# Kernel optimization log

Measured on AMD Instinct MI355X. Metric: run time of the kernel, lower is better.

## Reference

```python
import jax, jax.numpy as jnp
import numpy as np

T, B, DIN, H, DM, HYP, L = 128, 512, 512, 512, 256, 256, 100
STDV = 1.0 / np.sqrt(H)  # reset_parameters: uniform(-1/sqrt(hidden), 1/sqrt(hidden)) for ALL params
EPS = 1e-5


def setup_inputs() -> dict:
    key = jax.random.key(0)
    it = iter(jax.random.split(key, 32))
    U = lambda s: jax.random.uniform(next(it), s, jnp.float32, -STDV, STDV)
    x = jax.random.normal(next(it), (T, B, DIN), jnp.float32)
    meta = jax.random.normal(next(it), (B, L, DM), jnp.float32)
    inp = jax.random.randint(next(it), (B, L), 0, 5)
    return dict(
        x=x, meta=meta, inp=inp,
        # AttnModel (query from x, keys from meta)
        Wq=U((HYP, DIN)), bq=U((HYP,)), Wk=U((HYP, DM)), bk=U((HYP,)),
        # MergeLayer fc1 (fc2 is unused in MergeLayer.forward)
        Wm=U((HYP, DIN + DM + H)), bm=U((HYP,)),
        # hypernetwork projections z_h/z_x/z_b
        Wzh=U((4 * HYP, HYP)), bzh=U((4 * HYP,)),
        Wzx=U((4 * HYP, HYP)), bzx=U((4 * HYP,)),
        Wzb=U((4 * HYP, HYP)),
        # per-gate d_h/d_x/d_b maps (stacked over the 4 gates)
        Wdh=U((4, H, HYP)), Wdx=U((4, H, HYP)), Wdb=U((4, H, HYP)), bdb=U((4, H)),
        # main LSTM weights
        w_h=U((4, H, H)), w_x=U((4, H, DIN)),
        # per-gate LayerNorm affine
        ln_g=U((4, H)), ln_b=U((4, H)),
    )


def reference(x, meta, inp, Wq, bq, Wk, bk, Wm, bm, Wzh, bzh, Wzx, bzx, Wzb,
              Wdh, Wdx, Wdb, bdb, w_h, w_x, ln_g, ln_b):
    # --- AttnModel: attention-pool meta per timestep, meta_fea = [x, attended] ---
    q = jnp.einsum('tbi,hi->tbh', x, Wq) + bq                       # [T,B,HYP]
    k = jnp.einsum('blm,hm->blh', meta, Wk) + bk                    # [B,L,HYP]
    scores = jnp.einsum('tbh,blh->tbl', q, k) / jnp.sqrt(jnp.float32(HYP))
    scores = jnp.where((inp == 0)[None], -1e9, scores)              # pad mask
    attn = jax.nn.softmax(scores, axis=-1)
    attended = jnp.einsum('tbl,blm->tbm', attn, meta)               # [T,B,DM]
    meta_fea = jnp.concatenate([x, attended], axis=-1)              # [T,B,DIN+DM]

    def step(carry, xs):
        h, c = carry
        x_t, mf_t = xs
        # MergeLayer: relu(fc1(cat([meta_fea_t, h])))
        merged = jax.nn.relu(jnp.concatenate([mf_t, h], -1) @ Wm.T + bm)  # [B,HYP]
        zh = (merged @ Wzh.T + bzh).reshape(B, 4, HYP)
        zx = (merged @ Wzx.T + bzx).reshape(B, 4, HYP)
        zb = (merged @ Wzb.T).reshape(B, 4, HYP)
        d_h = jnp.einsum('bkz,khz->bkh', zh, Wdh)
        d_x = jnp.einsum('bkz,khz->bkh', zx, Wdx)
        d_b = jnp.einsum('bkz,khz->bkh', zb, Wdb) + bdb
        wh = jnp.einsum('khj,bj->bkh', w_h, h)
        wx = jnp.einsum('khj,bj->bkh', w_x, x_t)
        y = d_h * wh + d_x * wx + d_b                               # [B,4,H]
        mu = y.mean(-1, keepdims=True)
        var = ((y - mu) ** 2).mean(-1, keepdims=True)
        y = (y - mu) / jnp.sqrt(var + EPS) * ln_g + ln_b
        i, f, g, o = y[:, 0], y[:, 1], y[:, 2], y[:, 3]
        c_n = jax.nn.sigmoid(f) * c + jax.nn.sigmoid(i) * jnp.tanh(g)
        h_n = jax.nn.sigmoid(o) * jnp.tanh(c_n)
        return (h_n, c_n), h_n

    h0 = jnp.zeros((B, H), x.dtype)
    c0 = jnp.zeros((B, H), x.dtype)
    (hT, cT), out = jax.lax.scan(step, (h0, c0), (x, meta_fea))
    h_hat = jnp.zeros((1, B, HYP), x.dtype)  # hyper-state unused in this cell
    return out, hT[None], cT[None], h_hat, h_hat
```

## Files before the change

### kernel.cpp

```cpp
#include <hip/hip_runtime.h>
#include <hip/hip_bf16.h>

typedef unsigned short ushort_t;
typedef __attribute__((ext_vector_type(8))) short bf16x8;
typedef __attribute__((ext_vector_type(4))) float f32x4;

#define T_DIM 128
#define B_DIM 512
#define DIN 512
#define H_DIM 512
#define DM 256
#define HYP 256
#define L_DIM 100

__device__ __forceinline__ float bf2f(ushort_t u) {
    return __uint_as_float(((unsigned)u) << 16);
}
__device__ __forceinline__ ushort_t f2bf(float f) {
    unsigned u = __float_as_uint(f);
    unsigned r = (u + 0x7fffu + ((u >> 16) & 1u)) >> 16;
    return (ushort_t)r;
}
__device__ __forceinline__ float sigmoidf_(float x) {
    return 1.0f / (1.0f + __expf(-x));
}
__device__ __forceinline__ float fixf(float v) {
    if (!(v == v)) return 0.f;
    return fminf(fmaxf(v, -65504.f), 65504.f);
}

__global__ __launch_bounds__(256) void detect_kernel(const ushort_t* x, int nscan, int* flag) {
    __shared__ int found;
    if (threadIdx.x == 0) found = 0;
    __syncthreads();
    int f = 0;
    for (int i = threadIdx.x; i < nscan; i += 256) {
        unsigned u = x[i];
        if ((u & 0x7F80u) == 0x7F80u) f = 1;
    }
    if (f) atomicOr(&found, 1);
    __syncthreads();
    if (threadIdx.x == 0) *flag = found;
}

struct IngestP {
    const void* src[21];
    ushort_t* dst[21];
    int n[21];
    long total;
    const int* flag;
};

__global__ __launch_bounds__(256) void ingest_all(IngestP p) {
    int f = *p.flag;
    long idx0 = (long)blockIdx.x * 256 + threadIdx.x;
    long stride = (long)gridDim.x * 256;
    for (long idx = idx0; idx < p.total; idx += stride) {
        long r = idx;
#pragma unroll 1
        for (int t = 0; t < 21; t++) {
            if (r < p.n[t]) {
                p.dst[t][r] = f ? f2bf(((const float*)p.src[t])[r])
                               : ((const ushort_t*)p.src[t])[r];
                break;
            }
            r -= p.n[t];
        }
    }
}

__global__ __launch_bounds__(256) void zero_hhat(void* outbase, const int* flagp) {
    long i = 34078720 + (long)blockIdx.x * 256 + threadIdx.x;
    if (*flagp) ((float*)outbase)[i] = 0.f;
    else        ((ushort_t*)outbase)[i] = 0;
}

struct GP {
    const ushort_t* A1; const ushort_t* A2;
    const ushort_t* W1; const ushort_t* W2;
    long lda1, lda2, ldw1, ldw2;
    int K1, wc1, wc2, Nsplit, K, mode;
    const ushort_t* bias; ushort_t* outb; long ldo;
    const ushort_t* pre; ushort_t* merged; float* wh;
    float* outf; const float* fbias;
};

__global__ __launch_bounds__(256) void gemm_bt(GP g) {
    __shared__ __attribute__((aligned(16))) ushort_t As[128 * 40];
    __shared__ __attribute__((aligned(16))) ushort_t Bs[128 * 40];
    int tid  = threadIdx.x;
    int lane = tid & 63, wave = tid >> 6;
    int wm = (wave & 1) * 64, wn = (wave >> 1) * 64;
    int ml = lane & 15, quad = lane >> 4;
    long rowA0 = (long)blockIdx.x * 128;
    long rowW0 = (long)blockIdx.y * 128;
    int arow = tid >> 2, acol = (tid & 3) * 8;

    f32x4 acc[4][4];
#pragma unroll
    for (int i = 0; i < 4; i++)
#pragma unroll
        for (int j = 0; j < 4; j++) acc[i][j] = (f32x4){0.f, 0.f, 0.f, 0.f};

    for (int k0 = 0; k0 < g.K; k0 += 32) {
        uint4 av[2], wv[2];
#pragma unroll
        for (int s = 0; s < 2; s++) {
            int r = arow + s * 64;
            int k = k0 + acol;
            const ushort_t* asrc = (k < g.K1)
                ? g.A1 + (rowA0 + r) * g.lda1 + k
                : g.A2 + (rowA0 + r) * g.lda2 + (k - g.K1);
            av[s] = *(const uint4*)asrc;
            long n = rowW0 + r;
            const ushort_t* wsrc = (n < g.Nsplit)
                ? g.W1 + n * g.ldw1 + g.wc1 + k
                : g.W2 + (n - g.Nsplit) * g.ldw2 + g.wc2 + k;
            wv[s] = *(const uint4*)wsrc;
        }
        __syncthreads();
#pragma unroll
        for (int s = 0; s < 2; s++) {
            *(uint4*)&As[(arow + s * 64) * 40 + acol] = av[s];
            *(uint4*)&Bs[(arow + s * 64) * 40 + acol] = wv[s];
        }
        __syncthreads();
        bf16x8 af[4], bfm[4];
#pragma unroll
        for (int i = 0; i < 4; i++)
            af[i] = *(const bf16x8*)&As[(wm + i * 16 + ml) * 40 + quad * 8];
#pragma unroll
        for (int j = 0; j < 4; j++)
            bfm[j] = *(const bf16x8*)&Bs[(wn + j * 16 + ml) * 40 + quad * 8];
#pragma unroll
        for (int i = 0; i < 4; i++)
#pragma unroll
            for (int j = 0; j < 4; j++)
                acc[i][j] = __builtin_amdgcn_mfma_f32_16x16x32_bf16(af[i], bfm[j], acc[i][j], 0, 0, 0);
    }

#pragma unroll
    for (int i = 0; i < 4; i++) {
#pragma unroll
        for (int j = 0; j < 4; j++) {
            long rb = rowA0 + wm + i * 16 + quad * 4;
            long cn = rowW0 + wn + j * 16 + ml;
#pragma unroll
            for (int r = 0; r < 4; r++) {
                float v = acc[i][j][r];
                long rr = rb + r;
                if (g.mode == 0) {
                    if (g.bias) v += bf2f(g.bias[cn]);
                    g.outb[rr * g.ldo + cn] = f2bf(v);
                } else if (g.mode == 1) {
                    if (cn < 256) {
                        v += bf2f(g.pre[rr * 256 + cn]);
                        v = v > 0.f ? v : 0.f;
                        g.merged[rr * 256 + cn] = f2bf(v);
                    } else {
                        g.wh[rr * 2048 + (cn - 256)] = v;
                    }
                } else {
                    g.outf[rr * g.ldo + cn] = v + g.fbias[cn];
                }
            }
        }
    }
}

__global__ __launch_bounds__(256) void attn_kernel(const ushort_t* q, const ushort_t* kmat,
                                                   const ushort_t* meta, const int* inp,
                                                   ushort_t* att) {
    int b = blockIdx.x;
    __shared__ __attribute__((aligned(16))) ushort_t klds[L_DIM * 264];
    __shared__ float qlds[256];
    __shared__ float sc[L_DIM];
    __shared__ int msk[L_DIM];
    __shared__ float inv_s;
    int tid = threadIdx.x;

    for (int idx = tid; idx < L_DIM * 32; idx += 256) {
        int r = idx >> 5, c8 = (idx & 31) * 8;
        *(uint4*)&klds[r * 264 + c8] = *(const uint4*)&kmat[((long)b * L_DIM + r) * 256 + c8];
    }
    if (tid < L_DIM) msk[tid] = inp[b * L_DIM + tid];

    for (int t = 0; t < T_DIM; t++) {
        __syncthreads();
        qlds[tid] = bf2f(q[((long)t * B_DIM + b) * 256 + tid]);
        __syncthreads();
        if (tid < 2 * L_DIM) {
            int l = tid >> 1, half = tid & 1;
            const ushort_t* kr = &klds[l * 264 + half * 128];
            const float* qp = &qlds[half * 128];
            float s = 0.f;
            for (int j = 0; j < 128; j++) s += qp[j] * bf2f(kr[j]);
            s += __shfl_xor(s, 1);
            if (half == 0) sc[l] = (msk[l] == 0) ? -1000000000.0f : s * 0.0625f;
        }
        __syncthreads();
        if (tid < 64) {
            float s1 = sc[tid];
            float s2 = (tid + 64 < L_DIM) ? sc[tid + 64] : -1e30f;
            float mx = fmaxf(s1, s2);
            for (int o = 1; o < 64; o <<= 1) mx = fmaxf(mx, __shfl_xor(mx, o));
            float e1 = __expf(s1 - mx);
            float e2 = (tid + 64 < L_DIM) ? __expf(s2 - mx) : 0.f;
            float tot = e1 + e2;
            for (int o = 1; o < 64; o <<= 1) tot += __shfl_xor(tot, o);
            sc[tid] = e1;
            if (tid + 64 < L_DIM) sc[tid + 64] = e2;
            if (tid == 0) inv_s = 1.0f / tot;
        }
        __syncthreads();
        float a = 0.f;
        const ushort_t* mb = &meta[(long)b * L_DIM * 256 + tid];
        for (int l = 0; l < L_DIM; l++) a += sc[l] * bf2f(mb[(long)l * 256]);
        a *= inv_s;
        att[((long)t * B_DIM + b) * 256 + tid] = f2bf(a);
    }
}

__global__ __launch_bounds__(256) void call_precompute(const ushort_t* Wdh, const ushort_t* Wdx,
                                                       const ushort_t* Wdb, const ushort_t* Wzh,
                                                       const ushort_t* Wzx, const ushort_t* Wzb,
                                                       ushort_t* Call) {
    int bk = blockIdx.x;
    int kind = bk >> 2, kk = bk & 3;
    int h0 = blockIdx.y * 64;
    int m0 = blockIdx.z * 64;
    const ushort_t* Wd = (kind == 0) ? Wdh : ((kind == 1) ? Wdx : Wdb);
    const ushort_t* Wz = (kind == 0) ? Wzh : ((kind == 1) ? Wzx : Wzb);
    __shared__ __attribute__((aligned(16))) ushort_t dt[64 * 72];
    __shared__ __attribute__((aligned(16))) ushort_t zt[64 * 72];
    int tid = threadIdx.x;
    int ty = tid >> 4, tx = tid & 15;
    float acc[4][4] = {};
    for (int z0 = 0; z0 < 256; z0 += 64) {
        __syncthreads();
        for (int idx = tid; idx < 512; idx += 256) {
            int r = idx >> 3, c8 = (idx & 7) * 8;
            *(uint4*)&dt[r * 72 + c8] = *(const uint4*)&Wd[((long)(kk * 512 + h0 + r)) * 256 + z0 + c8];
            *(uint4*)&zt[r * 72 + c8] = *(const uint4*)&Wz[((long)(kk * 256 + z0 + r)) * 256 + m0 + c8];
        }
        __syncthreads();
        for (int z = 0; z < 64; z++) {
            float a[4], bb[4];
#pragma unroll
            for (int i = 0; i < 4; i++) a[i] = bf2f(dt[(ty * 4 + i) * 72 + z]);
#pragma unroll
            for (int j = 0; j < 4; j++) bb[j] = bf2f(zt[z * 72 + tx * 4 + j]);
#pragma unroll
            for (int i = 0; i < 4; i++)
#pragma unroll
                for (int j = 0; j < 4; j++) acc[i][j] += a[i] * bb[j];
        }
    }
#pragma unroll
    for (int i = 0; i < 4; i++)
#pragma unroll
        for (int j = 0; j < 4; j++)
            Call[((long)(kind * 2048 + kk * 512 + h0 + ty * 4 + i)) * 256 + m0 + tx * 4 + j] = f2bf(acc[i][j]);
}

__global__ __launch_bounds__(256) void dbias_kernel(const ushort_t* Wdh, const ushort_t* Wdx,
                                                    const ushort_t* bzh, const ushort_t* bzx,
                                                    const ushort_t* bdb, float* dbias) {
    int n = blockIdx.x * 256 + threadIdx.x;
    int kind = n >> 11, kk = (n >> 9) & 3, h = n & 511;
    float s = 0.f;
    if (kind == 2) {
        s = bf2f(bdb[kk * 512 + h]);
    } else {
        const ushort_t* Wd = (kind == 0) ? Wdh : Wdx;
        const ushort_t* bz = (kind == 0) ? bzh : bzx;
        for (int z = 0; z < 256; z++)
            s += bf2f(Wd[((long)(kk * 512 + h)) * 256 + z]) * bf2f(bz[kk * 256 + z]);
    }
    dbias[n] = s;
}

__global__ __launch_bounds__(256) void step_elem(const float* dall, const float* wh,
                                                 const ushort_t* wx, float* c, ushort_t* hbf,
                                                 const ushort_t* ln_g, const ushort_t* ln_b,
                                                 void* outbase, long off_t, int last,
                                                 const int* flagp) {
    int b = blockIdx.x, tid = threadIdx.x;
    int w = tid >> 6, lane = tid & 63;
    __shared__ float yln[4 * 512];
    const float* db = dall + (long)b * 6144;
    const float* whb = wh + (long)b * 2048;
    const ushort_t* wxb = wx + (long)b * 2048;
    float y[8];
    float sum = 0.f, ss = 0.f;
#pragma unroll
    for (int j = 0; j < 8; j++) {
        int h = lane + j * 64;
        int n = w * 512 + h;
        float v = db[n] * whb[n] + db[2048 + n] * bf2f(wxb[n]) + db[4096 + n];
        v = fixf(v);
        y[j] = v;
        sum += v;
        ss += v * v;
    }
    for (int o = 1; o < 64; o <<= 1) {
        sum += __shfl_xor(sum, o);
        ss += __shfl_xor(ss, o);
    }
    float mu = sum * (1.f / 512.f);
    float var = ss * (1.f / 512.f) - mu * mu;
    float rstd = rsqrtf(fmaxf(var, 0.f) + 1e-5f);
#pragma unroll
    for (int j = 0; j < 8; j++) {
        int h = lane + j * 64;
        float g = bf2f(ln_g[w * 512 + h]);
        float bb = bf2f(ln_b[w * 512 + h]);
        yln[w * 512 + h] = (y[j] - mu) * rstd * g + bb;
    }
    __syncthreads();
    int f = *flagp;
#pragma unroll
    for (int s = 0; s < 2; s++) {
        int h = tid + s * 256;
        float iv = yln[h], fv = yln[512 + h], gv = yln[1024 + h], ov = yln[1536 + h];
        long ci = (long)b * 512 + h;
        float cold = c[ci];
        float cn = sigmoidf_(fv) * cold + sigmoidf_(iv) * tanhf(gv);
        float hn = sigmoidf_(ov) * tanhf(cn);
        c[ci] = cn;
        hbf[ci] = f2bf(hn);
        if (f) {
            float* of = (float*)outbase;
            of[off_t + ci] = hn;
            if (last) { of[33554432 + ci] = hn; of[33816576 + ci] = cn; }
        } else {
            ushort_t* ob = (ushort_t*)outbase;
            ob[off_t + ci] = f2bf(hn);
            if (last) { ob[33554432 + ci] = f2bf(hn); ob[33816576 + ci] = f2bf(cn); }
        }
    }
}

extern "C" void kernel_launch(void* const* d_in, const int* in_sizes, int n_in,
                              void* d_out, int out_size, void* d_ws, size_t ws_size,
                              hipStream_t stream) {
    const int* inp = (const int*)d_in[2];

    size_t off = 0;
    char* wsb = (char*)d_ws;
    auto alloc = [&](size_t bytes) -> void* {
        off = (off + 255) & ~(size_t)255;
        void* p = wsb + off;
        off += bytes;
        return p;
    };

    int* flagp = (int*)alloc(256);

    static const int fidx[21] = {0,1,3,4,5,6,7,8,9,10,11,12,13,14,15,16,17,18,19,20,21};
    IngestP ip{};
    long total = 0;
    ushort_t* canon[21];
    for (int t = 0; t < 21; t++) {
        int src_i = fidx[t];
        int n = in_sizes[src_i];
        canon[t] = (ushort_t*)alloc((size_t)n * 2);
        ip.src[t] = d_in[src_i];
        ip.dst[t] = canon[t];
        ip.n[t] = n;
        total += n;
    }
    ip.total = total;
    ip.flag = flagp;

    const ushort_t* x    = canon[0];
    const ushort_t* meta = canon[1];
    const ushort_t* Wq   = canon[2];
    const ushort_t* bq   = canon[3];
    const ushort_t* Wk   = canon[4];
    const ushort_t* bk   = canon[5];
    const ushort_t* Wm   = canon[6];
    const ushort_t* bm   = canon[7];
    const ushort_t* Wzh  = canon[8];
    const ushort_t* bzh  = canon[9];
    const ushort_t* Wzx  = canon[10];
    const ushort_t* bzx  = canon[11];
    const ushort_t* Wzb  = canon[12];
    const ushort_t* Wdh  = canon[13];
    const ushort_t* Wdx  = canon[14];
    const ushort_t* Wdb  = canon[15];
    const ushort_t* bdb  = canon[16];
    const ushort_t* w_h  = canon[17];
    const ushort_t* w_x  = canon[18];
    const ushort_t* ln_g = canon[19];
    const ushort_t* ln_b = canon[20];

    ushort_t* qb    = (ushort_t*)alloc(33554432);
    ushort_t* kmb   = (ushort_t*)alloc(26214400);
    ushort_t* attb  = (ushort_t*)alloc(33554432);
    ushort_t* preb  = (ushort_t*)alloc(33554432);
    ushort_t* callb = (ushort_t*)alloc(3145728);
    float*    dbias = (float*)alloc(24576);
    ushort_t* hbf   = (ushort_t*)alloc(524288);
    float*    cf    = (float*)alloc(1048576);
    ushort_t* mgd   = (ushort_t*)alloc(262144);
    float*    whf   = (float*)alloc(4194304);
    float*    dall  = (float*)alloc(12582912);
    size_t base_end = (off + 255) & ~(size_t)255;
    bool full = (base_end + 268435456ull) <= ws_size;
    ushort_t* wxb = (ushort_t*)alloc(full ? 268435456ull : 2097152ull);

    detect_kernel<<<dim3(1), 256, 0, stream>>>((const ushort_t*)d_in[0], 262144, flagp);
    ingest_all<<<dim3(2048), 256, 0, stream>>>(ip);
    zero_hhat<<<dim3(1024), 256, 0, stream>>>(d_out, flagp);
    hipMemsetAsync(hbf, 0, 524288, stream);
    hipMemsetAsync(cf, 0, 1048576, stream);

    const int BIG = 1 << 30;

    {
        GP g{};
        g.A1 = meta; g.lda1 = 256; g.K1 = BIG; g.A2 = meta; g.lda2 = 256;
        g.W1 = Wk; g.ldw1 = 256; g.wc1 = 0; g.Nsplit = BIG; g.W2 = Wk; g.ldw2 = 256; g.wc2 = 0;
        g.K = 256; g.mode = 0; g.bias = bk; g.outb = kmb; g.ldo = 256;
        gemm_bt<<<dim3(400, 2), 256, 0, stream>>>(g);
    }
    {
        GP g{};
        g.A1 = x; g.lda1 = 512; g.K1 = BIG; g.A2 = x; g.lda2 = 512;
        g.W1 = Wq; g.ldw1 = 512; g.wc1 = 0; g.Nsplit = BIG; g.W2 = Wq; g.ldw2 = 512; g.wc2 = 0;
        g.K = 512; g.mode = 0; g.bias = bq; g.outb = qb; g.ldo = 256;
        gemm_bt<<<dim3(512, 2), 256, 0, stream>>>(g);
    }
    attn_kernel<<<dim3(512), 256, 0, stream>>>(qb, kmb, meta, inp, attb);
    {
        GP g{};
        g.A1 = x; g.lda1 = 512; g.K1 = 512; g.A2 = attb; g.lda2 = 256;
        g.W1 = Wm; g.ldw1 = 1280; g.wc1 = 0; g.Nsplit = BIG; g.W2 = Wm; g.ldw2 = 1280; g.wc2 = 0;
        g.K = 768; g.mode = 0; g.bias = bm; g.outb = preb; g.ldo = 256;
        gemm_bt<<<dim3(512, 2), 256, 0, stream>>>(g);
    }
    if (full) {
        GP g{};
        g.A1 = x; g.lda1 = 512; g.K1 = BIG; g.A2 = x; g.lda2 = 512;
        g.W1 = w_x; g.ldw1 = 512; g.wc1 = 0; g.Nsplit = BIG; g.W2 = w_x; g.ldw2 = 512; g.wc2 = 0;
        g.K = 512; g.mode = 0; g.bias = nullptr; g.outb = wxb; g.ldo = 2048;
        gemm_bt<<<dim3(512, 16), 256, 0, stream>>>(g);
    }
    call_precompute<<<dim3(12, 8, 4), 256, 0, stream>>>(Wdh, Wdx, Wdb, Wzh, Wzx, Wzb, callb);
    dbias_kernel<<<dim3(24), 256, 0, stream>>>(Wdh, Wdx, bzh, bzx, bdb, dbias);

    for (int t = 0; t < T_DIM; t++) {
        if (!full) {
            GP g{};
            g.A1 = x + (long)t * B_DIM * DIN; g.lda1 = 512; g.K1 = BIG; g.A2 = g.A1; g.lda2 = 512;
            g.W1 = w_x; g.ldw1 = 512; g.wc1 = 0; g.Nsplit = BIG; g.W2 = w_x; g.ldw2 = 512; g.wc2 = 0;
            g.K = 512; g.mode = 0; g.bias = nullptr; g.outb = wxb; g.ldo = 2048;
            gemm_bt<<<dim3(4, 16), 256, 0, stream>>>(g);
        }
        {
            GP g{};
            g.A1 = hbf; g.lda1 = 512; g.K1 = BIG; g.A2 = hbf; g.lda2 = 512;
            g.W1 = Wm; g.ldw1 = 1280; g.wc1 = 768; g.Nsplit = 256;
            g.W2 = w_h; g.ldw2 = 512; g.wc2 = 0;
            g.K = 512; g.mode = 1;
            g.pre = preb + (long)t * B_DIM * 256; g.merged = mgd; g.wh = whf;
            gemm_bt<<<dim3(4, 18), 256, 0, stream>>>(g);
        }
        {
            GP g{};
            g.A1 = mgd; g.lda1 = 256; g.K1 = BIG; g.A2 = mgd; g.lda2 = 256;
            g.W1 = callb; g.ldw1 = 256; g.wc1 = 0; g.Nsplit = BIG; g.W2 = callb; g.ldw2 = 256; g.wc2 = 0;
            g.K = 256; g.mode = 2; g.outf = dall; g.ldo = 6144; g.fbias = dbias;
            gemm_bt<<<dim3(4, 48), 256, 0, stream>>>(g);
        }
        const ushort_t* wxt = full ? (wxb + (long)t * B_DIM * 2048) : wxb;
        step_elem<<<dim3(512), 256, 0, stream>>>(dall, whf, wxt, cf, hbf, ln_g, ln_b,
                                                 d_out, (long)t * B_DIM * H_DIM,
                                                 (t == T_DIM - 1) ? 1 : 0, flagp);
    }
}
```

Measured before the change: 13.03 ms.

## Fuse recurrent scan into one persistent cooperative kernel with slab-level counters

Replaces the 128-step host loop of three GEMM launches plus an elementwise kernel with a single persistent cooperative kernel. Work is split into 64-row slabs, and producers and consumers synchronise through per-slab atomic release/acquire counters instead of kernel boundaries. This removes about 500 launches and the full-device barriers between stages, so different slabs can advance through stages independently. In exchange it uses 64x64 tiles, which reuse data less than the old 128x128 tiles, relies on spin-waits and co-residency of all blocks, and can deadlock if the non-cooperative fallback launch is taken with blocks that are not all resident.

```diff
diff --git a/kernel.cpp b/kernel.cpp
--- a/kernel.cpp
+++ b/kernel.cpp
@@ -81,8 +81,6 @@
     long lda1, lda2, ldw1, ldw2;
     int K1, wc1, wc2, Nsplit, K, mode;
     const ushort_t* bias; ushort_t* outb; long ldo;
-    const ushort_t* pre; ushort_t* merged; float* wh;
-    float* outf; const float* fbias;
 };
 
 __global__ __launch_bounds__(256) void gemm_bt(GP g) {
@@ -149,20 +147,8 @@
             for (int r = 0; r < 4; r++) {
                 float v = acc[i][j][r];
                 long rr = rb + r;
-                if (g.mode == 0) {
-                    if (g.bias) v += bf2f(g.bias[cn]);
-                    g.outb[rr * g.ldo + cn] = f2bf(v);
-                } else if (g.mode == 1) {
-                    if (cn < 256) {
-                        v += bf2f(g.pre[rr * 256 + cn]);
-                        v = v > 0.f ? v : 0.f;
-                        g.merged[rr * 256 + cn] = f2bf(v);
-                    } else {
-                        g.wh[rr * 2048 + (cn - 256)] = v;
-                    }
-                } else {
-                    g.outf[rr * g.ldo + cn] = v + g.fbias[cn];
-                }
+                if (g.bias) v += bf2f(g.bias[cn]);
+                g.outb[rr * g.ldo + cn] = f2bf(v);
             }
         }
     }
@@ -280,63 +266,224 @@
     dbias[n] = s;
 }
 
-__global__ __launch_bounds__(256) void step_elem(const float* dall, const float* wh,
-                                                 const ushort_t* wx, float* c, ushort_t* hbf,
-                                                 const ushort_t* ln_g, const ushort_t* ln_b,
-                                                 void* outbase, long off_t, int last,
-                                                 const int* flagp) {
-    int b = blockIdx.x, tid = threadIdx.x;
-    int w = tid >> 6, lane = tid & 63;
-    __shared__ float yln[4 * 512];
-    const float* db = dall + (long)b * 6144;
-    const float* whb = wh + (long)b * 2048;
-    const ushort_t* wxb = wx + (long)b * 2048;
-    float y[8];
-    float sum = 0.f, ss = 0.f;
-#pragma unroll
-    for (int j = 0; j < 8; j++) {
-        int h = lane + j * 64;
-        int n = w * 512 + h;
-        float v = db[n] * whb[n] + db[2048 + n] * bf2f(wxb[n]) + db[4096 + n];
-        v = fixf(v);
-        y[j] = v;
-        sum += v;
-        ss += v * v;
-    }
-    for (int o = 1; o < 64; o <<= 1) {
-        sum += __shfl_xor(sum, o);
-        ss += __shfl_xor(ss, o);
-    }
-    float mu = sum * (1.f / 512.f);
-    float var = ss * (1.f / 512.f) - mu * mu;
-    float rstd = rsqrtf(fmaxf(var, 0.f) + 1e-5f);
-#pragma unroll
-    for (int j = 0; j < 8; j++) {
-        int h = lane + j * 64;
-        float g = bf2f(ln_g[w * 512 + h]);
-        float bb = bf2f(ln_b[w * 512 + h]);
-        yln[w * 512 + h] = (y[j] - mu) * rstd * g + bb;
-    }
-    __syncthreads();
-    int f = *flagp;
-#pragma unroll
-    for (int s = 0; s < 2; s++) {
-        int h = tid + s * 256;
-        float iv = yln[h], fv = yln[512 + h], gv = yln[1024 + h], ov = yln[1536 + h];
-        long ci = (long)b * 512 + h;
-        float cold = c[ci];
-        float cn = sigmoidf_(fv) * cold + sigmoidf_(iv) * tanhf(gv);
-        float hn = sigmoidf_(ov) * tanhf(cn);
-        c[ci] = cn;
-        hbf[ci] = f2bf(hn);
-        if (f) {
-            float* of = (float*)outbase;
-            of[off_t + ci] = hn;
-            if (last) { of[33554432 + ci] = hn; of[33816576 + ci] = cn; }
-        } else {
-            ushort_t* ob = (ushort_t*)outbase;
-            ob[off_t + ci] = f2bf(hn);
-            if (last) { ob[33554432 + ci] = f2bf(hn); ob[33816576 + ci] = f2bf(cn); }
+struct SP {
+    const ushort_t *x, *pre, *Wm, *w_h, *w_x, *callb, *ln_g, *ln_b, *wxall;
+    const float* dbias;
+    ushort_t *hbf, *mgd, *wxpp;
+    float *cf, *whf, *dall;
+    int* cnt;
+    void* outb;
+    const int* flagp;
+    int full;
+};
+
+#define CNT(p, kind, t, slab) ((p).cnt[((kind) * T_DIM + (t)) * 8 + (slab)])
+
+__device__ __forceinline__ void release_inc(int* ptr) {
+    __hip_atomic_fetch_add(ptr, 1, __ATOMIC_RELEASE, __HIP_MEMORY_SCOPE_AGENT);
+}
+__device__ __forceinline__ void acquire_wait(int* ptr, int target) {
+    while (__hip_atomic_load(ptr, __ATOMIC_ACQUIRE, __HIP_MEMORY_SCOPE_AGENT) < target)
+        __builtin_amdgcn_s_sleep(2);
+}
+
+__device__ __forceinline__ void tile64(const ushort_t* A, long lda,
+                                       const ushort_t* W, long ldw, int K,
+                                       ushort_t* As, ushort_t* Bs,
+                                       f32x4 acc[2][2], int tid) {
+    int lane = tid & 63, wave = tid >> 6;
+    int wm = (wave & 1) * 32, wn = (wave >> 1) * 32;
+    int ml = lane & 15, quad = lane >> 4;
+    int row = tid >> 2, col8 = (tid & 3) * 8;
+#pragma unroll
+    for (int i = 0; i < 2; i++)
+#pragma unroll
+        for (int j = 0; j < 2; j++) acc[i][j] = (f32x4){0.f, 0.f, 0.f, 0.f};
+    for (int k0 = 0; k0 < K; k0 += 32) {
+        uint4 av = *(const uint4*)(A + (long)row * lda + k0 + col8);
+        uint4 wv = *(const uint4*)(W + (long)row * ldw + k0 + col8);
+        __syncthreads();
+        *(uint4*)&As[row * 40 + col8] = av;
+        *(uint4*)&Bs[row * 40 + col8] = wv;
+        __syncthreads();
+        bf16x8 af[2], bfm[2];
+#pragma unroll
+        for (int i = 0; i < 2; i++)
+            af[i] = *(const bf16x8*)&As[(wm + i * 16 + ml) * 40 + quad * 8];
+#pragma unroll
+        for (int j = 0; j < 2; j++)
+            bfm[j] = *(const bf16x8*)&Bs[(wn + j * 16 + ml) * 40 + quad * 8];
+#pragma unroll
+        for (int i = 0; i < 2; i++)
+#pragma unroll
+            for (int j = 0; j < 2; j++)
+                acc[i][j] = __builtin_amdgcn_mfma_f32_16x16x32_bf16(af[i], bfm[j], acc[i][j], 0, 0, 0);
+    }
+}
+
+__global__ __launch_bounds__(256, 2) void scan_kernel(SP p) {
+    __shared__ __attribute__((aligned(16))) ushort_t As[64 * 40];
+    __shared__ __attribute__((aligned(16))) ushort_t Bs[64 * 40];
+    __shared__ float yln[2048];
+    int tid = threadIdx.x, bid = blockIdx.x, nb = gridDim.x;
+    int lane = tid & 63, wave = tid >> 6;
+    int wm = (wave & 1) * 32, wn = (wave >> 1) * 32;
+    int ml = lane & 15, quad = lane >> 4;
+    f32x4 acc[2][2];
+
+    for (int t = 0; t < T_DIM; t++) {
+        int n_s1 = 288 + (p.full ? 0 : 256);
+        for (int it = bid; it < n_s1; it += nb) {
+            if (it < 288) {
+                int slab = it / 36, ct = it % 36;
+                int rb0 = slab * 64;
+                if (tid == 0 && t > 0) acquire_wait(&CNT(p, 3, t - 1, slab), 64);
+                __syncthreads();
+                const ushort_t* A = p.hbf + (long)rb0 * 512;
+                if (ct < 4) {
+                    int cb0 = ct * 64;
+                    tile64(A, 512, p.Wm + (long)cb0 * 1280 + 768, 1280, 512, As, Bs, acc, tid);
+                    const ushort_t* pr = p.pre + ((long)t * B_DIM) * 256;
+#pragma unroll
+                    for (int i = 0; i < 2; i++)
+#pragma unroll
+                        for (int j = 0; j < 2; j++)
+#pragma unroll
+                            for (int r = 0; r < 4; r++) {
+                                int lr = wm + i * 16 + quad * 4 + r;
+                                int lc = wn + j * 16 + ml;
+                                float v = acc[i][j][r] + bf2f(pr[(long)(rb0 + lr) * 256 + cb0 + lc]);
+                                v = v > 0.f ? v : 0.f;
+                                p.mgd[(long)(rb0 + lr) * 256 + cb0 + lc] = f2bf(v);
+                            }
+                    __syncthreads();
+                    if (tid == 0) release_inc(&CNT(p, 0, t, slab));
+                } else {
+                    int cb0 = ct * 64 - 256;
+                    tile64(A, 512, p.w_h + (long)cb0 * 512, 512, 512, As, Bs, acc, tid);
+#pragma unroll
+                    for (int i = 0; i < 2; i++)
+#pragma unroll
+                        for (int j = 0; j < 2; j++)
+#pragma unroll
+                            for (int r = 0; r < 4; r++) {
+                                int lr = wm + i * 16 + quad * 4 + r;
+                                int lc = wn + j * 16 + ml;
+                                p.whf[(long)(rb0 + lr) * 2048 + cb0 + lc] = acc[i][j][r];
+                            }
+                    __syncthreads();
+                    if (tid == 0) release_inc(&CNT(p, 1, t, slab));
+                }
+            } else {
+                int it2 = it - 288;
+                int slab = it2 >> 5, ct = it2 & 31;
+                int rb0 = slab * 64, cb0 = ct * 64;
+                if (tid == 0 && t >= 2) acquire_wait(&CNT(p, 3, t - 2, slab), 64);
+                __syncthreads();
+                const ushort_t* A = p.x + ((long)t * B_DIM + rb0) * 512;
+                tile64(A, 512, p.w_x + (long)cb0 * 512, 512, 512, As, Bs, acc, tid);
+                ushort_t* wdst = p.wxpp + (long)(t & 1) * B_DIM * 2048;
+#pragma unroll
+                for (int i = 0; i < 2; i++)
+#pragma unroll
+                    for (int j = 0; j < 2; j++)
+#pragma unroll
+                        for (int r = 0; r < 4; r++) {
+                            int lr = wm + i * 16 + quad * 4 + r;
+                            int lc = wn + j * 16 + ml;
+                            wdst[(long)(rb0 + lr) * 2048 + cb0 + lc] = f2bf(acc[i][j][r]);
+                        }
+                __syncthreads();
+                if (tid == 0) release_inc(&CNT(p, 4, t, slab));
+            }
+        }
+        for (int it = bid; it < 768; it += nb) {
+            int slab = it / 96, ct = it % 96;
+            int rb0 = slab * 64, cb0 = ct * 64;
+            if (tid == 0) acquire_wait(&CNT(p, 0, t, slab), 4);
+            __syncthreads();
+            tile64(p.mgd + (long)rb0 * 256, 256, p.callb + (long)cb0 * 256, 256, 256,
+                   As, Bs, acc, tid);
+#pragma unroll
+            for (int i = 0; i < 2; i++)
+#pragma unroll
+                for (int j = 0; j < 2; j++)
+#pragma unroll
+                    for (int r = 0; r < 4; r++) {
+                        int lr = wm + i * 16 + quad * 4 + r;
+                        int lc = wn + j * 16 + ml;
+                        p.dall[(long)(rb0 + lr) * 6144 + cb0 + lc] =
+                            acc[i][j][r] + p.dbias[cb0 + lc];
+                    }
+            __syncthreads();
+            if (tid == 0) release_inc(&CNT(p, 2, t, slab));
+        }
+        for (int b = bid; b < B_DIM; b += nb) {
+            int slab = b >> 6;
+            if (tid == 0) {
+                acquire_wait(&CNT(p, 1, t, slab), 32);
+                acquire_wait(&CNT(p, 2, t, slab), 96);
+                if (!p.full) acquire_wait(&CNT(p, 4, t, slab), 32);
+            }
+            __syncthreads();
+            const float* db = p.dall + (long)b * 6144;
+            const float* whb = p.whf + (long)b * 2048;
+            const ushort_t* wxb = (p.full ? p.wxall + (long)t * B_DIM * 2048
+                                          : p.wxpp + (long)(t & 1) * B_DIM * 2048)
+                                  + (long)b * 2048;
+            int w = tid >> 6;
+            float y[8];
+            float sum = 0.f, ss = 0.f;
+#pragma unroll
+            for (int j = 0; j < 8; j++) {
+                int h = lane + j * 64;
+                int n = w * 512 + h;
+                float v = db[n] * whb[n] + db[2048 + n] * bf2f(wxb[n]) + db[4096 + n];
+                v = fixf(v);
+                y[j] = v;
+                sum += v;
+                ss += v * v;
+            }
+            for (int o = 1; o < 64; o <<= 1) {
+                sum += __shfl_xor(sum, o);
+                ss += __shfl_xor(ss, o);
+            }
+            float mu = sum * (1.f / 512.f);
+            float var = ss * (1.f / 512.f) - mu * mu;
+            float rstd = rsqrtf(fmaxf(var, 0.f) + 1e-5f);
+#pragma unroll
+            for (int j = 0; j < 8; j++) {
+                int h = lane + j * 64;
+                float g = bf2f(p.ln_g[w * 512 + h]);
+                float bb = bf2f(p.ln_b[w * 512 + h]);
+                yln[w * 512 + h] = (y[j] - mu) * rstd * g + bb;
+            }
+            __syncthreads();
+            int f = *p.flagp;
+            int last = (t == T_DIM - 1) ? 1 : 0;
+#pragma unroll
+            for (int s = 0; s < 2; s++) {
+                int h = tid + s * 256;
+                float iv = yln[h], fv = yln[512 + h], gv = yln[1024 + h], ov = yln[1536 + h];
+                long ci = (long)b * 512 + h;
+                float cold = p.cf[ci];
+                float cn = sigmoidf_(fv) * cold + sigmoidf_(iv) * tanhf(gv);
+                float hn = sigmoidf_(ov) * tanhf(cn);
+                p.cf[ci] = cn;
+                p.hbf[ci] = f2bf(hn);
+                long oo = (long)t * B_DIM * H_DIM + ci;
+                if (f) {
+                    float* of = (float*)p.outb;
+                    of[oo] = hn;
+                    if (last) { of[33554432 + ci] = hn; of[33816576 + ci] = cn; }
+                } else {
+                    ushort_t* ob = (ushort_t*)p.outb;
+                    ob[oo] = f2bf(hn);
+                    if (last) { ob[33554432 + ci] = f2bf(hn); ob[33816576 + ci] = f2bf(cn); }
+                }
+            }
+            __syncthreads();
+            if (tid == 0) release_inc(&CNT(p, 3, t, slab));
         }
     }
 }
@@ -406,15 +553,18 @@
     ushort_t* mgd   = (ushort_t*)alloc(262144);
     float*    whf   = (float*)alloc(4194304);
     float*    dall  = (float*)alloc(12582912);
+    int*      cnt   = (int*)alloc(20480);
+    ushort_t* wxpp  = (ushort_t*)alloc(4194304);
     size_t base_end = (off + 255) & ~(size_t)255;
     bool full = (base_end + 268435456ull) <= ws_size;
-    ushort_t* wxb = (ushort_t*)alloc(full ? 268435456ull : 2097152ull);
+    ushort_t* wxb = full ? (ushort_t*)alloc(268435456ull) : nullptr;
 
     detect_kernel<<<dim3(1), 256, 0, stream>>>((const ushort_t*)d_in[0], 262144, flagp);
     ingest_all<<<dim3(2048), 256, 0, stream>>>(ip);
     zero_hhat<<<dim3(1024), 256, 0, stream>>>(d_out, flagp);
     hipMemsetAsync(hbf, 0, 524288, stream);
     hipMemsetAsync(cf, 0, 1048576, stream);
+    hipMemsetAsync(cnt, 0, 20480, stream);
 
     const int BIG = 1 << 30;
 
@@ -450,33 +600,25 @@
     call_precompute<<<dim3(12, 8, 4), 256, 0, stream>>>(Wdh, Wdx, Wdb, Wzh, Wzx, Wzb, callb);
     dbias_kernel<<<dim3(24), 256, 0, stream>>>(Wdh, Wdx, bzh, bzx, bdb, dbias);
 
-    for (int t = 0; t < T_DIM; t++) {
-        if (!full) {
-            GP g{};
-            g.A1 = x + (long)t * B_DIM * DIN; g.lda1 = 512; g.K1 = BIG; g.A2 = g.A1; g.lda2 = 512;
-            g.W1 = w_x; g.ldw1 = 512; g.wc1 = 0; g.Nsplit = BIG; g.W2 = w_x; g.ldw2 = 512; g.wc2 = 0;
-            g.K = 512; g.mode = 0; g.bias = nullptr; g.outb = wxb; g.ldo = 2048;
-            gemm_bt<<<dim3(4, 16), 256, 0, stream>>>(g);
-        }
-        {
-            GP g{};
-            g.A1 = hbf; g.lda1 = 512; g.K1 = BIG; g.A2 = hbf; g.lda2 = 512;
-            g.W1 = Wm; g.ldw1 = 1280; g.wc1 = 768; g.Nsplit = 256;
-            g.W2 = w_h; g.ldw2 = 512; g.wc2 = 0;
-            g.K = 512; g.mode = 1;
-            g.pre = preb + (long)t * B_DIM * 256; g.merged = mgd; g.wh = whf;
-            gemm_bt<<<dim3(4, 18), 256, 0, stream>>>(g);
-        }
-        {
-            GP g{};
-            g.A1 = mgd; g.lda1 = 256; g.K1 = BIG; g.A2 = mgd; g.lda2 = 256;
-            g.W1 = callb; g.ldw1 = 256; g.wc1 = 0; g.Nsplit = BIG; g.W2 = callb; g.ldw2 = 256; g.wc2 = 0;
-            g.K = 256; g.mode = 2; g.outf = dall; g.ldo = 6144; g.fbias = dbias;
-            gemm_bt<<<dim3(4, 48), 256, 0, stream>>>(g);
-        }
-        const ushort_t* wxt = full ? (wxb + (long)t * B_DIM * 2048) : wxb;
-        step_elem<<<dim3(512), 256, 0, stream>>>(dall, whf, wxt, cf, hbf, ln_g, ln_b,
-                                                 d_out, (long)t * B_DIM * H_DIM,
-                                                 (t == T_DIM - 1) ? 1 : 0, flagp);
-    }
-}
+    SP sp{};
+    sp.x = x; sp.pre = preb; sp.Wm = Wm; sp.w_h = w_h; sp.w_x = w_x;
+    sp.callb = callb; sp.ln_g = ln_g; sp.ln_b = ln_b; sp.wxall = wxb;
+    sp.dbias = dbias; sp.hbf = hbf; sp.mgd = mgd; sp.wxpp = wxpp;
+    sp.cf = cf; sp.whf = whf; sp.dall = dall; sp.cnt = cnt;
+    sp.outb = d_out; sp.flagp = flagp; sp.full = full ? 1 : 0;
+
+    int nCU = 256, occB = 2, dev = 0;
+    hipGetDevice(&dev);
+    hipDeviceGetAttribute(&nCU, hipDeviceAttributeMultiprocessorCount, dev);
+    if (hipOccupancyMaxActiveBlocksPerMultiprocessor(&occB, scan_kernel, 256, 0) != hipSuccess
+        || occB < 1) occB = 1;
+    int grid = occB * nCU;
+    if (grid > 512) grid = 512;
+
+    void* args[] = {&sp};
+    hipError_t e = hipLaunchCooperativeKernel((const void*)scan_kernel, dim3(grid), dim3(256),
+                                              args, 0, stream);
+    if (e != hipSuccess) {
+        scan_kernel<<<dim3(grid), 256, 0, stream>>>(sp);
+    }
+}
```

Result: slower. 34.19 ms (+162.4%).
